# Kernel tuning notes

Hardware: AMD Instinct MI355X
Metric: run time of the kernel (lower is better)

Reference implementation:

```python
import jax, jax.numpy as jnp
import numpy as np

NEG_INF = -1e30  # stand-in for -inf that is safe under fp16/bf16 softmax


def setup_inputs() -> dict:
    key = jax.random.key(0)
    k1, k2, k3, k4 = jax.random.split(key, 4)
    B, S, D_IN, D_OUT = 4, 4096, 2048, 2048
    x = jax.random.normal(k1, (B, S, D_IN), dtype=jnp.float32)
    scale = 0.02
    Wq = jax.random.normal(k2, (D_IN, D_OUT), dtype=jnp.float32) * scale
    Wk = jax.random.normal(k3, (D_IN, D_OUT), dtype=jnp.float32) * scale
    Wv = jax.random.normal(k4, (D_IN, D_OUT), dtype=jnp.float32) * scale
    return {"x": x, "Wq": Wq, "Wk": Wk, "Wv": Wv}


def reference(x, Wq, Wk, Wv):
    # x: [B, S, d_in]; Wq/Wk/Wv: [d_in, d_out] (torch Linear weight transposed)
    B, S, _ = x.shape
    q = jnp.einsum('bsd,de->bse', x, Wq)
    k = jnp.einsum('bsd,de->bse', x, Wk)
    v = jnp.einsum('bsd,de->bse', x, Wv)
    d_k = k.shape[-1]
    scale = 1.0 / jnp.sqrt(jnp.asarray(d_k, dtype=x.dtype))
    # attn_scores[b, i, j] = q_i . k_j
    scores = jnp.einsum('bqe,bke->bqk', q, k) * scale
    # causal mask: position i attends to j <= i
    i = jnp.arange(S)[:, None]
    j = jnp.arange(S)[None, :]
    scores = jnp.where(j > i, NEG_INF, scores)
    attn = jax.nn.softmax(scores, axis=-1)
    # dropout p=0.0 / eval mode -> identity
    return jnp.einsum('bqk,bke->bqe', attn, v)
```

## Files before the change

kernel.cpp:

```cpp
#include <hip/hip_runtime.h>

using u16   = unsigned short;
using s16x8 = __attribute__((ext_vector_type(8))) short;
using u16x8 = __attribute__((ext_vector_type(8))) unsigned short;
using f32x4 = __attribute__((ext_vector_type(4))) float;

__device__ __forceinline__ u16 f2bf(float f) {
    unsigned u = __float_as_uint(f);
    u += 0x7FFFu + ((u >> 16) & 1u);
    return (u16)(u >> 16);
}

__device__ __forceinline__ void gload16(const void* g, void* l) {
    __builtin_amdgcn_global_load_lds((const __attribute__((address_space(1))) void*)g,
                                     (__attribute__((address_space(3))) void*)l, 16, 0, 0);
}

#define MFMA_BF16(a, b, d) \
    d = __builtin_amdgcn_mfma_f32_16x16x32_bf16(a, b, d, 0, 0, 0)

__device__ __forceinline__ void gemm256_core(
    const u16* __restrict__ A, const u16* __restrict__ Bt,
    int lda, int ldb, int kSteps, u16* lds, f32x4 (&acc)[8][4])
{
    const int tid  = threadIdx.x;
    const int lane = tid & 63;
    const int wid  = tid >> 6;
    const int wr   = wid >> 2;
    const int wc   = wid & 3;
    const int c    = lane & 15;
    const int g    = lane >> 4;

    const int srow = tid >> 3;
    const int scol = ((tid & 7) * 8) ^ ((srow & 7) << 3);
    const u16* pA = A  + (size_t)srow * lda + scol;
    const u16* pB = Bt + (size_t)srow * ldb + scol;
    const size_t sA = (size_t)64 * lda;
    const size_t sB = (size_t)64 * ldb;
    const int ldst = tid * 8;

    const int low0 = (g * 8)      ^ ((c & 7) << 3);
    const int low1 = (32 + g * 8) ^ ((c & 7) << 3);
    const int aRow = (wr * 128 + c) * 64;
    const int bRow = (wc * 64 + c) * 64;

#pragma unroll
    for (int s = 0; s < 4; ++s) {
        gload16(pA + s * sA, lds + s * 4096 + ldst);
        gload16(pB + s * sB, lds + 16384 + s * 4096 + ldst);
    }
    if (kSteps > 1) { pA += 64; pB += 64; }

    for (int t = 0; t < kSteps; ++t) {
        const u16* rdA = lds + (t & 1) * 32768;
        const u16* rdB = rdA + 16384;
        u16* wA = lds + ((t & 1) ^ 1) * 32768;
        u16* wB = wA + 16384;

        s16x8 av[4][2], bv[2][2], bw[2][2];

        gload16(pA,      wA + ldst);
        gload16(pA + sA, wA + 4096 + ldst);
        asm volatile("s_waitcnt vmcnt(2)" ::: "memory");
        __builtin_amdgcn_s_barrier();
        __builtin_amdgcn_sched_barrier(0);
#pragma unroll
        for (int m = 0; m < 4; ++m) {
            av[m][0] = *(const s16x8*)(rdA + aRow + m * 1024 + low0);
            av[m][1] = *(const s16x8*)(rdA + aRow + m * 1024 + low1);
        }
#pragma unroll
        for (int n = 0; n < 2; ++n) {
            bv[n][0] = *(const s16x8*)(rdB + bRow + n * 1024 + low0);
            bv[n][1] = *(const s16x8*)(rdB + bRow + n * 1024 + low1);
        }
        __builtin_amdgcn_s_setprio(1);
#pragma unroll
        for (int m = 0; m < 4; ++m)
#pragma unroll
            for (int n = 0; n < 2; ++n) {
                MFMA_BF16(av[m][0], bv[n][0], acc[m][n]);
                MFMA_BF16(av[m][1], bv[n][1], acc[m][n]);
            }
        __builtin_amdgcn_s_setprio(0);
        __builtin_amdgcn_s_barrier();

#pragma unroll
        for (int n = 0; n < 2; ++n) {
            bw[n][0] = *(const s16x8*)(rdB + bRow + (n + 2) * 1024 + low0);
            bw[n][1] = *(const s16x8*)(rdB + bRow + (n + 2) * 1024 + low1);
        }
        gload16(pA + 2 * sA, wA + 8192 + ldst);
        gload16(pA + 3 * sA, wA + 12288 + ldst);
        __builtin_amdgcn_sched_barrier(0);
        __builtin_amdgcn_s_barrier();
        __builtin_amdgcn_s_setprio(1);
#pragma unroll
        for (int m = 0; m < 4; ++m)
#pragma unroll
            for (int n = 0; n < 2; ++n) {
                MFMA_BF16(av[m][0], bw[n][0], acc[m][n + 2]);
                MFMA_BF16(av[m][1], bw[n][1], acc[m][n + 2]);
            }
        __builtin_amdgcn_s_setprio(0);
        __builtin_amdgcn_s_barrier();

#pragma unroll
        for (int m = 0; m < 4; ++m) {
            av[m][0] = *(const s16x8*)(rdA + aRow + (m + 4) * 1024 + low0);
            av[m][1] = *(const s16x8*)(rdA + aRow + (m + 4) * 1024 + low1);
        }
        gload16(pB,      wB + ldst);
        gload16(pB + sB, wB + 4096 + ldst);
        __builtin_amdgcn_sched_barrier(0);
        __builtin_amdgcn_s_barrier();
        __builtin_amdgcn_s_setprio(1);
#pragma unroll
        for (int m = 0; m < 4; ++m)
#pragma unroll
            for (int n = 0; n < 2; ++n) {
                MFMA_BF16(av[m][0], bw[n][0], acc[m + 4][n + 2]);
                MFMA_BF16(av[m][1], bw[n][1], acc[m + 4][n + 2]);
            }
        __builtin_amdgcn_s_setprio(0);
        __builtin_amdgcn_s_barrier();

        gload16(pB + 2 * sB, wB + 8192 + ldst);
        gload16(pB + 3 * sB, wB + 12288 + ldst);
        __builtin_amdgcn_sched_barrier(0);
        __builtin_amdgcn_s_barrier();
        __builtin_amdgcn_s_setprio(1);
#pragma unroll
        for (int m = 0; m < 4; ++m)
#pragma unroll
            for (int n = 0; n < 2; ++n) {
                MFMA_BF16(av[m][0], bv[n][0], acc[m + 4][n]);
                MFMA_BF16(av[m][1], bv[n][1], acc[m + 4][n]);
            }
        __builtin_amdgcn_s_setprio(0);
        __builtin_amdgcn_s_barrier();

        const int adv = (t + 2 < kSteps) ? 64 : 0;
        pA += adv; pB += adv;
    }
    asm volatile("s_waitcnt vmcnt(0)" ::: "memory");
}

__device__ __forceinline__ int xcd_swz(int bid, int nwg) {
    return (bid & 7) * (nwg >> 3) + (bid >> 3);
}

__global__ __launch_bounds__(512, 2) void gemm256_bf16(
    const u16* __restrict__ A, const u16* __restrict__ Bt, u16* __restrict__ C,
    int N, int K, long aBatch, long bBatch, long cBatch)
{
    __shared__ u16 lds[65536];
    const int bid = xcd_swz((int)blockIdx.x, (int)gridDim.x);
    const int nT = N >> 8;
    const int m0 = (bid / nT) << 8;
    const int n0 = (bid % nT) << 8;
    const int b  = blockIdx.z;
    const u16* Ab = A  + (size_t)b * aBatch + (size_t)m0 * K;
    const u16* Bb = Bt + (size_t)b * bBatch + (size_t)n0 * K;
    f32x4 acc[8][4] = {};
    gemm256_core(Ab, Bb, K, K, K >> 6, lds, acc);

    u16* Cb = C + (size_t)b * cBatch;
    const int lane = threadIdx.x & 63;
    const int c = lane & 15, g = lane >> 4;
    const int wid = threadIdx.x >> 6;
    const int rowb = m0 + (wid >> 2) * 128 + g * 4;
    const int colb = n0 + (wid & 3) * 64 + c;
#pragma unroll
    for (int m = 0; m < 8; ++m)
#pragma unroll
        for (int n = 0; n < 4; ++n)
#pragma unroll
            for (int r = 0; r < 4; ++r)
                Cb[(size_t)(rowb + m * 16 + r) * N + colb + n * 16] = f2bf(acc[m][n][r]);
}

__global__ __launch_bounds__(512, 2) void attn_score256(
    const u16* __restrict__ Tm, const u16* __restrict__ Xb,
    u16* __restrict__ P, float* __restrict__ L, long pStride, int bBase)
{
    __shared__ u16 lds[65536];
    const int b  = bBase + blockIdx.z;
    const int wg = xcd_swz((int)blockIdx.x, (int)gridDim.x);
    int it = (int)((sqrtf(8.0f * (float)wg + 1.0f) - 1.0f) * 0.5f);
    while ((it + 1) * (it + 2) / 2 <= wg) ++it;
    while (it * (it + 1) / 2 > wg) --it;
    const int jt = wg - it * (it + 1) / 2;
    const int i0 = it << 8, j0 = jt << 8;

    const u16* Ab = Tm + ((size_t)b * 4096 + i0) * 2048;
    const u16* Bb = Xb + ((size_t)b * 4096 + j0) * 2048;
    f32x4 acc[8][4] = {};
    gemm256_core(Ab, Bb, 2048, 2048, 32, lds, acc);

    u16*   Pb = P + (size_t)blockIdx.z * pStride;
    float* Lb = L + (size_t)b * 4096;
    const int lane = threadIdx.x & 63;
    const int c = lane & 15, g = lane >> 4;
    const int wid = threadIdx.x >> 6;
    const int rowb = i0 + (wid >> 2) * 128 + g * 4;
    const int colb = j0 + (wid & 3) * 64 + c;
    const float SCALE = 0.022097086912079608f;

    float rsum[8][4];
#pragma unroll
    for (int m = 0; m < 8; ++m)
#pragma unroll
        for (int r = 0; r < 4; ++r) rsum[m][r] = 0.0f;
#pragma unroll
    for (int m = 0; m < 8; ++m) {
#pragma unroll
        for (int r = 0; r < 4; ++r) {
            const int Ig = rowb + m * 16 + r;
#pragma unroll
            for (int n = 0; n < 4; ++n) {
                const int Jg = colb + n * 16;
                float p = (Jg > Ig) ? 0.0f : __expf(acc[m][n][r] * SCALE);
                Pb[(size_t)Ig * 4096 + Jg] = f2bf(p);
                rsum[m][r] += p;
            }
        }
    }
#pragma unroll
    for (int m = 0; m < 8; ++m)
#pragma unroll
        for (int r = 0; r < 4; ++r) {
            float v = rsum[m][r];
            v += __shfl_xor(v, 1);
            v += __shfl_xor(v, 2);
            v += __shfl_xor(v, 4);
            v += __shfl_xor(v, 8);
            rsum[m][r] = v;
        }
    if (c == 0) {
#pragma unroll
        for (int m = 0; m < 8; ++m)
#pragma unroll
            for (int r = 0; r < 4; ++r)
                atomicAdd(&Lb[rowb + m * 16 + r], rsum[m][r]);
    }
}

__global__ __launch_bounds__(512, 2) void attn_pv256(
    const u16* __restrict__ P, const u16* __restrict__ Vt,
    const float* __restrict__ L, float* __restrict__ Out, long pStride, int bBase)
{
    __shared__ u16 lds[65536];
    const int b   = bBase + blockIdx.z;
    const int idx = xcd_swz((int)blockIdx.x, (int)gridDim.x);
    const int it  = 15 - (idx >> 3);
    const int nt  = idx & 7;
    const int i0 = it << 8, n0 = nt << 8;

    const u16* Ab = P  + (size_t)blockIdx.z * pStride + (size_t)i0 * 4096;
    const u16* Bb = Vt + (size_t)b * (2048ll * 4096) + (size_t)n0 * 4096;
    f32x4 acc[8][4] = {};
    gemm256_core(Ab, Bb, 4096, 4096, (it + 1) * 4, lds, acc);

    const float* Lb = L + (size_t)b * 4096;
    float* Ob = Out + (size_t)b * (4096ll * 2048);
    const int lane = threadIdx.x & 63;
    const int c = lane & 15, g = lane >> 4;
    const int wid = threadIdx.x >> 6;
    const int rowb = i0 + (wid >> 2) * 128 + g * 4;
    const int colb = n0 + (wid & 3) * 64 + c;
#pragma unroll
    for (int m = 0; m < 8; ++m) {
#pragma unroll
        for (int r = 0; r < 4; ++r) {
            const int I = rowb + m * 16 + r;
            const float inv = 1.0f / Lb[I];
#pragma unroll
            for (int n = 0; n < 4; ++n)
                Ob[(size_t)I * 2048 + colb + n * 16] = acc[m][n][r] * inv;
        }
    }
}

__device__ __forceinline__ void gemm_core_128(
    const u16* __restrict__ A, const u16* __restrict__ Bt,
    int lda, int ldb, int kSteps,
    u16* ldsA, u16* ldsB, f32x4 (&acc)[4][4])
{
    const int tid  = threadIdx.x;
    const int lane = tid & 63;
    const int wr   = (tid >> 7) & 1;
    const int wc   = (tid >> 6) & 1;
    const int g    = lane >> 4;
    const int c    = lane & 15;

    const u16* aSrc = A  + (size_t)(tid >> 3) * lda + (tid & 7) * 8;
    const u16* bSrc = Bt + (size_t)(tid >> 3) * ldb + (tid & 7) * 8;
    u16* aDst = ldsA + tid * 8;
    u16* bDst = ldsB + tid * 8;

    for (int kt = 0; kt < kSteps; ++kt) {
#pragma unroll
        for (int it = 0; it < 4; ++it) {
            gload16(aSrc + (size_t)it * 32 * lda, aDst + it * 2048);
            gload16(bSrc + (size_t)it * 32 * ldb, bDst + it * 2048);
        }
        aSrc += 64; bSrc += 64;
        __syncthreads();
#pragma unroll
        for (int kk = 0; kk < 2; ++kk) {
            s16x8 av[4], bv[4];
#pragma unroll
            for (int m = 0; m < 4; ++m)
                av[m] = *(const s16x8*)(ldsA + (size_t)(wr*64 + m*16 + c) * 64 + kk*32 + g*8);
#pragma unroll
            for (int n = 0; n < 4; ++n)
                bv[n] = *(const s16x8*)(ldsB + (size_t)(wc*64 + n*16 + c) * 64 + kk*32 + g*8);
#pragma unroll
            for (int m = 0; m < 4; ++m)
#pragma unroll
                for (int n = 0; n < 4; ++n)
                    MFMA_BF16(av[m], bv[n], acc[m][n]);
        }
        __syncthreads();
    }
}

__global__ __launch_bounds__(256) void gemm_bt_bf16(
    const u16* __restrict__ A, const u16* __restrict__ Bt, u16* __restrict__ C,
    int N, int K)
{
    __shared__ u16 ldsA[128 * 64];
    __shared__ u16 ldsB[128 * 64];
    const int nT = N >> 7;
    const int m0 = (int)(blockIdx.x / nT) << 7;
    const int n0 = (int)(blockIdx.x % nT) << 7;
    const u16* Ab = A + (size_t)m0 * K;
    const u16* Bb = Bt + (size_t)n0 * K;
    f32x4 acc[4][4] = {};
    gemm_core_128(Ab, Bb, K, K, K >> 6, ldsA, ldsB, acc);

    const int lane = threadIdx.x & 63;
    const int wr = (threadIdx.x >> 7) & 1, wc = (threadIdx.x >> 6) & 1;
    const int rb = m0 + wr * 64 + ((lane >> 4) << 2);
    const int cb = n0 + wc * 64 + (lane & 15);
#pragma unroll
    for (int m = 0; m < 4; ++m)
#pragma unroll
        for (int n = 0; n < 4; ++n)
#pragma unroll
            for (int r = 0; r < 4; ++r)
                C[(size_t)(rb + m*16 + r) * N + cb + n*16] = f2bf(acc[m][n][r]);
}

__global__ __launch_bounds__(256) void cvt_f32_bf16x8(
    const float* __restrict__ in, u16* __restrict__ out, long n8)
{
    long i = (long)blockIdx.x * 256 + threadIdx.x;
    if (i >= n8) return;
    const float4* p = (const float4*)(in + i * 8);
    float4 v0 = p[0], v1 = p[1];
    u16x8 o;
    o[0] = f2bf(v0.x); o[1] = f2bf(v0.y); o[2] = f2bf(v0.z); o[3] = f2bf(v0.w);
    o[4] = f2bf(v1.x); o[5] = f2bf(v1.y); o[6] = f2bf(v1.z); o[7] = f2bf(v1.w);
    *(u16x8*)(out + i * 8) = o;
}

__global__ __launch_bounds__(256) void transpose_cvt(
    const float* __restrict__ W, u16* __restrict__ Wt, int dim)
{
    __shared__ float tile[64][65];
    const int nb = dim >> 6;
    const int br = blockIdx.x / nb, bc = blockIdx.x % nb;
    const int t  = threadIdx.x;
    const int lr = t >> 2;
    const int lc = (t & 3) << 4;
    const float* src = W + (size_t)(br * 64 + lr) * dim + bc * 64 + lc;
#pragma unroll
    for (int q = 0; q < 4; ++q) {
        float4 v = *(const float4*)(src + q * 4);
        tile[lr][lc + q * 4 + 0] = v.x;
        tile[lr][lc + q * 4 + 1] = v.y;
        tile[lr][lc + q * 4 + 2] = v.z;
        tile[lr][lc + q * 4 + 3] = v.w;
    }
    __syncthreads();
    u16* dst = Wt + (size_t)(bc * 64 + lr) * dim + br * 64 + lc;
    u16x8 o0, o1;
#pragma unroll
    for (int q = 0; q < 8; ++q) o0[q] = f2bf(tile[lc + q][lr]);
#pragma unroll
    for (int q = 0; q < 8; ++q) o1[q] = f2bf(tile[lc + 8 + q][lr]);
    *(u16x8*)(dst)     = o0;
    *(u16x8*)(dst + 8) = o1;
}

__global__ __launch_bounds__(256) void zero_f32(float* p, int n)
{
    int i = blockIdx.x * 256 + threadIdx.x;
    if (i < n) p[i] = 0.0f;
}

extern "C" void kernel_launch(void* const* d_in, const int* in_sizes, int n_in,
                              void* d_out, int out_size, void* d_ws, size_t ws_size,
                              hipStream_t stream)
{
    const float* x  = (const float*)d_in[0];
    const float* Wq = (const float*)d_in[1];
    const float* Wk = (const float*)d_in[2];
    const float* Wv = (const float*)d_in[3];
    float* out = (float*)d_out;

    char* ws = (char*)d_ws;
    u16*   xb  = (u16*)(ws + 0ull);
    u16*   Tm  = (u16*)(ws + 67108864ull);
    u16*   Vt  = (u16*)(ws + 134217728ull);
    u16*   Wqb = (u16*)(ws + 201326592ull);
    u16*   Wkb = (u16*)(ws + 209715200ull);
    u16*   Wvt = (u16*)(ws + 218103808ull);
    u16*   Mt  = (u16*)(ws + 226492416ull);
    float* L   = (float*)(ws + 234881024ull);
    u16*   P   = (u16*)(ws + 234946560ull);
    const size_t needBase = 234946560ull;
    const size_t needFull = needBase + 134217728ull;
    const size_t needPerB = needBase + 33554432ull;
    if (ws_size < needPerB) return;

    cvt_f32_bf16x8<<<16384, 256, 0, stream>>>(x,  xb,  4194304);
    cvt_f32_bf16x8<<<2048,  256, 0, stream>>>(Wq, Wqb, 524288);
    cvt_f32_bf16x8<<<2048,  256, 0, stream>>>(Wk, Wkb, 524288);
    transpose_cvt <<<1024,  256, 0, stream>>>(Wv, Wvt, 2048);

    gemm_bt_bf16<<<dim3(256, 1, 1), 256, 0, stream>>>(Wkb, Wqb, Mt, 2048, 2048);
    gemm256_bf16<<<dim3(512, 1, 1), 512, 0, stream>>>(xb, Mt, Tm, 2048, 2048, 0, 0, 0);
    gemm256_bf16<<<dim3(128, 1, 4), 512, 0, stream>>>(Wvt, xb, Vt, 4096, 2048,
                                                      0, 8388608, 8388608);
    zero_f32<<<64, 256, 0, stream>>>(L, 16384);

    if (ws_size >= needFull) {
        attn_score256<<<dim3(136, 1, 4), 512, 0, stream>>>(Tm, xb, P, L, 16777216ll, 0);
        attn_pv256   <<<dim3(128, 1, 4), 512, 0, stream>>>(P, Vt, L, out, 16777216ll, 0);
    } else {
        for (int b = 0; b < 4; ++b) {
            attn_score256<<<dim3(136, 1, 1), 512, 0, stream>>>(Tm, xb, P, L, 0, b);
            attn_pv256   <<<dim3(128, 1, 1), 512, 0, stream>>>(P, Vt, L, out, 0, b);
        }
    }
}
```

Measured before the change: 732.8 us.

## Rework GEMM prefetch schedule and rebalance causal PV tile ordering across XCDs

Result: faster. 640.9 us (-12.5%).

```diff
diff --git a/kernel.cpp b/kernel.cpp
--- a/kernel.cpp
+++ b/kernel.cpp
@@ -44,10 +44,17 @@
     const int aRow = (wr * 128 + c) * 64;
     const int bRow = (wc * 64 + c) * 64;
 
-#pragma unroll
-    for (int s = 0; s < 4; ++s) {
-        gload16(pA + s * sA, lds + s * 4096 + ldst);
-        gload16(pB + s * sB, lds + 16384 + s * 4096 + ldst);
+    {
+        u16* wA = lds;
+        u16* wB = lds + 16384;
+        gload16(pA + 0 * sA, wA + 0 * 4096 + ldst);
+        gload16(pA + 2 * sA, wA + 2 * 4096 + ldst);
+        gload16(pB + 0 * sB, wB + 0 * 4096 + ldst);
+        gload16(pB + 1 * sB, wB + 1 * 4096 + ldst);
+        gload16(pB + 2 * sB, wB + 2 * 4096 + ldst);
+        gload16(pB + 3 * sB, wB + 3 * 4096 + ldst);
+        gload16(pA + 1 * sA, wA + 1 * 4096 + ldst);
+        gload16(pA + 3 * sA, wA + 3 * 4096 + ldst);
     }
     if (kSteps > 1) { pA += 64; pB += 64; }
 
@@ -56,14 +63,21 @@
         const u16* rdB = rdA + 16384;
         u16* wA = lds + ((t & 1) ^ 1) * 32768;
         u16* wB = wA + 16384;
+        const bool more = (t + 1 < kSteps);
 
         s16x8 av[4][2], bv[2][2], bw[2][2];
 
-        gload16(pA,      wA + ldst);
-        gload16(pA + sA, wA + 4096 + ldst);
         asm volatile("s_waitcnt vmcnt(2)" ::: "memory");
         __builtin_amdgcn_s_barrier();
         __builtin_amdgcn_sched_barrier(0);
+        if (more) {
+            gload16(pA + 0 * sA, wA + 0 * 4096 + ldst);
+            gload16(pA + 2 * sA, wA + 2 * 4096 + ldst);
+            gload16(pB + 0 * sB, wB + 0 * 4096 + ldst);
+            gload16(pB + 1 * sB, wB + 1 * 4096 + ldst);
+            gload16(pB + 2 * sB, wB + 2 * 4096 + ldst);
+            gload16(pB + 3 * sB, wB + 3 * 4096 + ldst);
+        }
 #pragma unroll
         for (int m = 0; m < 4; ++m) {
             av[m][0] = *(const s16x8*)(rdA + aRow + m * 1024 + low0);
@@ -90,10 +104,10 @@
             bw[n][0] = *(const s16x8*)(rdB + bRow + (n + 2) * 1024 + low0);
             bw[n][1] = *(const s16x8*)(rdB + bRow + (n + 2) * 1024 + low1);
         }
-        gload16(pA + 2 * sA, wA + 8192 + ldst);
-        gload16(pA + 3 * sA, wA + 12288 + ldst);
-        __builtin_amdgcn_sched_barrier(0);
-        __builtin_amdgcn_s_barrier();
+        if (more) {
+            gload16(pA + 1 * sA, wA + 1 * 4096 + ldst);
+            gload16(pA + 3 * sA, wA + 3 * 4096 + ldst);
+        }
         __builtin_amdgcn_s_setprio(1);
 #pragma unroll
         for (int m = 0; m < 4; ++m)
@@ -103,17 +117,16 @@
                 MFMA_BF16(av[m][1], bw[n][1], acc[m][n + 2]);
             }
         __builtin_amdgcn_s_setprio(0);
+
+        if (more) asm volatile("s_waitcnt vmcnt(8)" ::: "memory");
+        else      asm volatile("s_waitcnt vmcnt(0)" ::: "memory");
         __builtin_amdgcn_s_barrier();
-
+        __builtin_amdgcn_sched_barrier(0);
 #pragma unroll
         for (int m = 0; m < 4; ++m) {
             av[m][0] = *(const s16x8*)(rdA + aRow + (m + 4) * 1024 + low0);
             av[m][1] = *(const s16x8*)(rdA + aRow + (m + 4) * 1024 + low1);
         }
-        gload16(pB,      wB + ldst);
-        gload16(pB + sB, wB + 4096 + ldst);
-        __builtin_amdgcn_sched_barrier(0);
-        __builtin_amdgcn_s_barrier();
         __builtin_amdgcn_s_setprio(1);
 #pragma unroll
         for (int m = 0; m < 4; ++m)
@@ -125,10 +138,6 @@
         __builtin_amdgcn_s_setprio(0);
         __builtin_amdgcn_s_barrier();
 
-        gload16(pB + 2 * sB, wB + 8192 + ldst);
-        gload16(pB + 3 * sB, wB + 12288 + ldst);
-        __builtin_amdgcn_sched_barrier(0);
-        __builtin_amdgcn_s_barrier();
         __builtin_amdgcn_s_setprio(1);
 #pragma unroll
         for (int m = 0; m < 4; ++m)
@@ -138,10 +147,8 @@
                 MFMA_BF16(av[m][1], bv[n][1], acc[m + 4][n]);
             }
         __builtin_amdgcn_s_setprio(0);
-        __builtin_amdgcn_s_barrier();
-
-        const int adv = (t + 2 < kSteps) ? 64 : 0;
-        pA += adv; pB += adv;
+
+        if (t + 2 < kSteps) { pA += 64; pB += 64; }
     }
     asm volatile("s_waitcnt vmcnt(0)" ::: "memory");
 }
@@ -248,16 +255,23 @@
 
 __global__ __launch_bounds__(512, 2) void attn_pv256(
     const u16* __restrict__ P, const u16* __restrict__ Vt,
-    const float* __restrict__ L, float* __restrict__ Out, long pStride, int bBase)
+    const float* __restrict__ L, float* __restrict__ Out,
+    long pStride, int bBase, int zCount)
 {
     __shared__ u16 lds[65536];
-    const int b   = bBase + blockIdx.z;
-    const int idx = xcd_swz((int)blockIdx.x, (int)gridDim.x);
-    const int it  = 15 - (idx >> 3);
-    const int nt  = idx & 7;
+    const int d = (int)blockIdx.x;
+    const int x = d & 7;
+    const int q = d >> 3;
+    const int spr = zCount << 3;
+    const int s = q % spr;
+    const int r = q / spr;
+    const int nt = s & 7;
+    const int z  = s >> 3;
+    const int it = r ? x : 15 - x;
+    const int b  = bBase + z;
     const int i0 = it << 8, n0 = nt << 8;
 
-    const u16* Ab = P  + (size_t)blockIdx.z * pStride + (size_t)i0 * 4096;
+    const u16* Ab = P  + (size_t)z * pStride + (size_t)i0 * 4096;
     const u16* Bb = Vt + (size_t)b * (2048ll * 4096) + (size_t)n0 * 4096;
     f32x4 acc[8][4] = {};
     gemm256_core(Ab, Bb, 4096, 4096, (it + 1) * 4, lds, acc);
@@ -272,12 +286,12 @@
 #pragma unroll
     for (int m = 0; m < 8; ++m) {
 #pragma unroll
-        for (int r = 0; r < 4; ++r) {
-            const int I = rowb + m * 16 + r;
+        for (int r2 = 0; r2 < 4; ++r2) {
+            const int I = rowb + m * 16 + r2;
             const float inv = 1.0f / Lb[I];
 #pragma unroll
             for (int n = 0; n < 4; ++n)
-                Ob[(size_t)I * 2048 + colb + n * 16] = acc[m][n][r] * inv;
+                Ob[(size_t)I * 2048 + colb + n * 16] = acc[m][n][r2] * inv;
         }
     }
 }
@@ -439,11 +453,11 @@
 
     if (ws_size >= needFull) {
         attn_score256<<<dim3(136, 1, 4), 512, 0, stream>>>(Tm, xb, P, L, 16777216ll, 0);
-        attn_pv256   <<<dim3(128, 1, 4), 512, 0, stream>>>(P, Vt, L, out, 16777216ll, 0);
+        attn_pv256   <<<dim3(512, 1, 1), 512, 0, stream>>>(P, Vt, L, out, 16777216ll, 0, 4);
     } else {
         for (int b = 0; b < 4; ++b) {
             attn_score256<<<dim3(136, 1, 1), 512, 0, stream>>>(Tm, xb, P, L, 0, b);
-            attn_pv256   <<<dim3(128, 1, 1), 512, 0, stream>>>(P, Vt, L, out, 0, b);
-        }
-    }
-}
+            attn_pv256   <<<dim3(128, 1, 1), 512, 0, stream>>>(P, Vt, L, out, 0, b, 1);
+        }
+    }
+}
```
